# Performance work log

Measured on AMD Instinct MI355X. Metric: run time of the kernel, lower is better.

The kernel has to match this reference:

```python
import jax, jax.numpy as jnp
import numpy as np

E = 1024          # n_embed_dim
H = 64            # head_size = n_embed_dim // n_heads (16)

def setup_inputs() -> dict:
    key = jax.random.key(0)
    k_x, k_q, k_k, k_v = jax.random.split(key, 4)
    scale = 1.0 / np.sqrt(E)
    return {
        "x": jax.random.normal(k_x, (4, 2048, E), dtype=jnp.float32),
        "ln_gamma": jnp.ones((E,), jnp.float32),
        "ln_beta": jnp.zeros((E,), jnp.float32),
        # torch nn.Linear weights: [out_features, in_features]
        "Wq": jax.random.normal(k_q, (H, E), dtype=jnp.float32) * scale,
        "Wk": jax.random.normal(k_k, (H, E), dtype=jnp.float32) * scale,
        "Wv": jax.random.normal(k_v, (H, E), dtype=jnp.float32) * scale,
    }

def reference(x, ln_gamma, ln_beta, Wq, Wk, Wv):
    # LayerNorm over last dim (eps matches torch default 1e-5)
    mu = jnp.mean(x, axis=-1, keepdims=True)
    var = jnp.mean(jnp.square(x - mu), axis=-1, keepdims=True)
    xn = (x - mu) * jax.lax.rsqrt(var + 1e-5) * ln_gamma + ln_beta

    q = jnp.einsum('bse,he->bsh', xn, Wq)   # [B,S,H]
    k = jnp.einsum('bse,he->bsh', xn, Wk)
    v = jnp.einsum('bse,he->bsh', xn, Wv)

    scores = jnp.einsum('bqh,bkh->bqk', q, k) / jnp.sqrt(jnp.float32(H))
    S = x.shape[1]
    causal = jnp.tril(jnp.ones((S, S), dtype=bool))
    scores = jnp.where(causal, scores, -jnp.inf)
    attn = jax.nn.softmax(scores, axis=-1)
    return jnp.einsum('bqk,bkh->bqh', attn, v)
```

## Files before the change

kernel.cpp:

```cpp
#include <hip/hip_runtime.h>

#define E 1024
#define HH 64
#define BB 4
#define SS 2048
#define BS (BB*SS)
#define NSLOT 144

typedef unsigned short u16;
typedef short bf16x8 __attribute__((ext_vector_type(8)));
typedef float f32x4 __attribute__((ext_vector_type(4)));

#define LOG2E_O8 0.18033688011112042f

__device__ inline u16 f2bf(float f) {
    unsigned int u = __float_as_uint(f);
    unsigned int r = (u + 0x7FFFu + ((u >> 16) & 1u)) >> 16;
    return (u16)r;
}
__device__ inline float bf2f(u16 h) {
    return __uint_as_float(((unsigned int)h) << 16);
}

__global__ __launch_bounds__(256) void ln_wcast(const float* __restrict__ x,
        const float* __restrict__ gamma, const float* __restrict__ beta,
        const float* __restrict__ Wq, const float* __restrict__ Wk,
        const float* __restrict__ Wv,
        u16* __restrict__ xn, u16* __restrict__ wc) {
    const int t = threadIdx.x;
    if (blockIdx.x < 2048) {
        const int w = t >> 6, lane = t & 63;
        const size_t row = (size_t)blockIdx.x * 4 + w;
        const float4* xr = (const float4*)(x + row * E);
        float4 v[4];
        #pragma unroll
        for (int i = 0; i < 4; ++i) v[i] = xr[lane + 64 * i];
        float s = 0.f, sq = 0.f;
        #pragma unroll
        for (int i = 0; i < 4; ++i) {
            s  += v[i].x + v[i].y + v[i].z + v[i].w;
            sq += v[i].x*v[i].x + v[i].y*v[i].y + v[i].z*v[i].z + v[i].w*v[i].w;
        }
        #pragma unroll
        for (int off = 32; off > 0; off >>= 1) {
            s  += __shfl_xor(s,  off);
            sq += __shfl_xor(sq, off);
        }
        const float mean = s * (1.0f / E);
        const float var  = sq * (1.0f / E) - mean * mean;
        const float rstd = rsqrtf(var + 1e-5f);
        const float4* gr = (const float4*)gamma;
        const float4* br = (const float4*)beta;
        #pragma unroll
        for (int i = 0; i < 4; ++i) {
            const float4 g  = gr[lane + 64 * i];
            const float4 bt = br[lane + 64 * i];
            ushort4 o;
            o.x = f2bf((v[i].x - mean) * rstd * g.x + bt.x);
            o.y = f2bf((v[i].y - mean) * rstd * g.y + bt.y);
            o.z = f2bf((v[i].z - mean) * rstd * g.z + bt.z);
            o.w = f2bf((v[i].w - mean) * rstd * g.w + bt.w);
            *(ushort4*)(xn + row * E + (lane + 64 * i) * 4) = o;
        }
    } else {
        const int row = blockIdx.x - 2048;
        const float* src = (row < 64)  ? (Wq + (size_t)row * E)
                         : (row < 128) ? (Wk + (size_t)(row - 64) * E)
                                       : (Wv + (size_t)(row - 128) * E);
        const float sc = (row < 64) ? LOG2E_O8 : 1.0f;
        const float4 v = *(const float4*)(src + t * 4);
        ushort4 o;
        o.x = f2bf(v.x * sc); o.y = f2bf(v.y * sc);
        o.z = f2bf(v.z * sc); o.w = f2bf(v.w * sc);
        *(ushort4*)(wc + (size_t)row * E + t * 4) = o;
    }
}

__global__ __launch_bounds__(256) void qkv_mfma(const u16* __restrict__ xn,
        const u16* __restrict__ wc,
        u16* __restrict__ qb, u16* __restrict__ kb, u16* __restrict__ vt) {
    const int mb   = blockIdx.x >> 1;
    const int half = blockIdx.x & 1;
    const int row0 = mb * 32;
    const int t = threadIdx.x;
    const int w = t >> 6, lane = t & 63;
    const int quad = lane >> 4, r15 = lane & 15;
    const int mt = w >> 1, cgrp = w & 1;
    __shared__ u16 Xs[32 * 128];
    __shared__ u16 Ws[96 * 128];
    f32x4 acc[3] = {};
    const int xrow = mt * 16 + r15;

    for (int kc8 = 0; kc8 < 8; ++kc8) {
        __syncthreads();
        {
            const int row = t >> 3, ch = t & 7;
            #pragma unroll
            for (int hf = 0; hf < 2; ++hf) {
                const uint4 d = *(const uint4*)(xn + (size_t)(row0 + row) * E
                                                + kc8 * 128 + hf * 64 + ch * 8);
                *(uint4*)&Xs[row * 128 + hf * 64 + (ch ^ (row & 7)) * 8] = d;
            }
        }
        #pragma unroll
        for (int i = 0; i < 6; ++i) {
            const int idx = i * 256 + t;
            const int wl = idx >> 4, ch16 = idx & 15;
            const int hf = ch16 >> 3, ch = ch16 & 7;
            const uint4 d = *(const uint4*)(wc + (size_t)(half * 96 + wl) * E
                                            + kc8 * 128 + hf * 64 + ch * 8);
            *(uint4*)&Ws[wl * 128 + hf * 64 + (ch ^ (wl & 7)) * 8] = d;
        }
        __syncthreads();
        #pragma unroll
        for (int kk = 0; kk < 4; ++kk) {
            const int hf = kk >> 1, q4 = (kk & 1) * 4 + quad;
            const bf16x8 af = *(const bf16x8*)&Xs[xrow * 128 + hf * 64 + (q4 ^ (xrow & 7)) * 8];
            #pragma unroll
            for (int j = 0; j < 3; ++j) {
                const int wl = (cgrp * 3 + j) * 16 + r15;
                const bf16x8 bfr = *(const bf16x8*)&Ws[wl * 128 + hf * 64 + (q4 ^ (wl & 7)) * 8];
                acc[j] = __builtin_amdgcn_mfma_f32_16x16x32_bf16(af, bfr, acc[j], 0, 0, 0);
            }
        }
    }
    const int b    = row0 >> 11;
    const int key0 = row0 & 2047;
    #pragma unroll
    for (int j = 0; j < 3; ++j) {
        const int cg  = half * 96 + cgrp * 48 + j * 16 + r15;
        const int sel = cg >> 6;
        const int col = cg & 63;
        if (sel < 2) {
            u16* base = (sel == 0) ? qb : kb;
            #pragma unroll
            for (int r = 0; r < 4; ++r) {
                const size_t row = (size_t)row0 + mt * 16 + quad * 4 + r;
                base[row * HH + col] = f2bf(acc[j][r]);
            }
        } else {
            ushort4 pk;
            pk.x = f2bf(acc[j][0]); pk.y = f2bf(acc[j][1]);
            pk.z = f2bf(acc[j][2]); pk.w = f2bf(acc[j][3]);
            *(ushort4*)(vt + (size_t)b * HH * SS + (size_t)col * SS
                           + key0 + mt * 16 + quad * 4) = pk;
        }
    }
}

__global__ __launch_bounds__(256) void attn_partial(const u16* __restrict__ qb,
        const u16* __restrict__ kb, const u16* __restrict__ vt,
        u16* __restrict__ po, float* __restrict__ pl,
        float* __restrict__ out) {
    const int bid = blockIdx.x;
    const int b   = bid >> 8;
    const int rem = bid & 255;
    const int qt  = rem >> 3, c = rem & 7;
    const int a   = qt >> 2;
    if (c > a) return;
    const int nc   = a + 1;
    const int r_   = qt & 3;
    const int slot = b * NSLOT + 2 * a * (a + 1) + r_ * (a + 1) + c;
    const int q0   = qt << 6;
    const int t = threadIdx.x;
    const int w = t >> 6, lane = t & 63;
    const int quad = lane >> 4, r15 = lane & 15;

    __shared__ u16 Ks[4 * 64 * 64];
    __shared__ u16 VT[4 * 64 * 64];
    __shared__ u16 Ps[64 * 64];

    const size_t qrow = ((size_t)b * SS + q0 + w * 16 + r15) * HH;
    const bf16x8 qf0 = *(const bf16x8*)(qb + qrow + quad * 8);
    const bf16x8 qf1 = *(const bf16x8*)(qb + qrow + 32 + quad * 8);

    const int ntiles = min(c * 4 + 4, qt + 1) - c * 4;

    {
        const int row = t >> 2, ch0 = (t & 3) * 2;
        for (int tl = 0; tl < ntiles; ++tl) {
            const int kt = (c * 4 + tl) << 6;
            const uint4* srcK = (const uint4*)(kb + ((size_t)b * SS + kt + row) * HH + ch0 * 8);
            const uint4 k0 = srcK[0], k1 = srcK[1];
            *(uint4*)&Ks[tl * 4096 + row * 64 + ((ch0    ) ^ (row & 7)) * 8] = k0;
            *(uint4*)&Ks[tl * 4096 + row * 64 + ((ch0 + 1) ^ (row & 7)) * 8] = k1;
            const uint4* srcV = (const uint4*)(vt + (size_t)b * HH * SS + (size_t)row * SS
                                               + kt + ch0 * 8);
            const uint4 v0 = srcV[0], v1 = srcV[1];
            *(uint4*)&VT[tl * 4096 + row * 64 + ((ch0    ) ^ (row & 7)) * 8] = v0;
            *(uint4*)&VT[tl * 4096 + row * 64 + ((ch0 + 1) ^ (row & 7)) * 8] = v1;
        }
    }
    __syncthreads();

    f32x4 o[4] = {};
    float l_[4] = {0.f, 0.f, 0.f, 0.f};

    for (int tl = 0; tl < ntiles; ++tl) {
        const int tile = c * 4 + tl;
        const u16* KsT = &Ks[tl * 4096];
        const u16* VTT = &VT[tl * 4096];

        f32x4 s[4] = {};
        #pragma unroll
        for (int nt = 0; nt < 4; ++nt) {
            const int krow = nt * 16 + r15;
            const bf16x8 k0 = *(const bf16x8*)&KsT[krow * 64 + ((    quad) ^ (krow & 7)) * 8];
            const bf16x8 k1 = *(const bf16x8*)&KsT[krow * 64 + ((4 + quad) ^ (krow & 7)) * 8];
            s[nt] = __builtin_amdgcn_mfma_f32_16x16x32_bf16(qf0, k0, s[nt], 0, 0, 0);
            s[nt] = __builtin_amdgcn_mfma_f32_16x16x32_bf16(qf1, k1, s[nt], 0, 0, 0);
        }
        if (tile == qt) {
            #pragma unroll
            for (int nt = 0; nt < 4; ++nt)
                #pragma unroll
                for (int r = 0; r < 4; ++r)
                    if (nt * 16 + r15 > w * 16 + quad * 4 + r) s[nt][r] = -INFINITY;
        }

        float p[4][4];
        #pragma unroll
        for (int r = 0; r < 4; ++r) {
            #pragma unroll
            for (int nt = 0; nt < 4; ++nt)
                p[nt][r] = __builtin_amdgcn_exp2f(s[nt][r]);
            l_[r] += (p[0][r] + p[1][r]) + (p[2][r] + p[3][r]);
        }

        #pragma unroll
        for (int nt = 0; nt < 4; ++nt)
            #pragma unroll
            for (int r = 0; r < 4; ++r) {
                const int prow = w * 16 + quad * 4 + r;
                const int col  = nt * 16 + r15;
                Ps[prow * 64 + (((col >> 3) ^ (prow & 7)) * 8) + (col & 7)] = f2bf(p[nt][r]);
            }
        const int arow = w * 16 + r15;
        const bf16x8 pf0 = *(const bf16x8*)&Ps[arow * 64 + ((    quad) ^ (arow & 7)) * 8];
        const bf16x8 pf1 = *(const bf16x8*)&Ps[arow * 64 + ((4 + quad) ^ (arow & 7)) * 8];

        #pragma unroll
        for (int ht = 0; ht < 4; ++ht) {
            const int vrow = ht * 16 + r15;
            const bf16x8 v0 = *(const bf16x8*)&VTT[vrow * 64 + ((    quad) ^ (vrow & 7)) * 8];
            const bf16x8 v1 = *(const bf16x8*)&VTT[vrow * 64 + ((4 + quad) ^ (vrow & 7)) * 8];
            o[ht] = __builtin_amdgcn_mfma_f32_16x16x32_bf16(pf0, v0, o[ht], 0, 0, 0);
            o[ht] = __builtin_amdgcn_mfma_f32_16x16x32_bf16(pf1, v1, o[ht], 0, 0, 0);
        }
    }

    #pragma unroll
    for (int r = 0; r < 4; ++r) {
        l_[r] += __shfl_xor(l_[r], 1); l_[r] += __shfl_xor(l_[r], 2);
        l_[r] += __shfl_xor(l_[r], 4); l_[r] += __shfl_xor(l_[r], 8);
    }

    if (nc == 1) {
        #pragma unroll
        for (int r = 0; r < 4; ++r) {
            const float inv = 1.0f / l_[r];
            const size_t orow = ((size_t)b * SS + q0 + w * 16 + quad * 4 + r) * HH;
            #pragma unroll
            for (int ht = 0; ht < 4; ++ht)
                out[orow + ht * 16 + r15] = o[ht][r] * inv;
        }
        return;
    }
    #pragma unroll
    for (int r = 0; r < 4; ++r) {
        const int q = w * 16 + quad * 4 + r;
        #pragma unroll
        for (int ht = 0; ht < 4; ++ht)
            po[(size_t)slot * 4096 + q * 64 + ht * 16 + r15] = f2bf(o[ht][r]);
        if (r15 == 0) pl[slot * 64 + q] = l_[r];
    }
}

__global__ __launch_bounds__(256) void attn_reduce(const u16* __restrict__ po,
        const float* __restrict__ pl, float* __restrict__ out) {
    const int bid = blockIdx.x;
    const int b = bid >> 7, rem = bid & 127;
    const int qt = rem >> 2, qq = rem & 3;
    if (qt < 4) return;
    const int a = qt >> 2, r_ = qt & 3;
    const int nc = a + 1;
    const int sbase = b * NSLOT + 2 * a * (a + 1) + r_ * (a + 1);
    const int t = threadIdx.x;
    const int h = t & 63, qr = t >> 6;
    #pragma unroll
    for (int i = 0; i < 4; ++i) {
        const int q = qq * 16 + qr * 4 + i;
        float osum = 0.f, lsum = 0.f;
        for (int cidx = 0; cidx < nc; ++cidx) {
            osum += bf2f(po[(size_t)(sbase + cidx) * 4096 + q * 64 + h]);
            lsum += pl[(sbase + cidx) * 64 + q];
        }
        out[((size_t)b * SS + (qt << 6) + q) * HH + h] = osum / lsum;
    }
}

extern "C" void kernel_launch(void* const* d_in, const int* in_sizes, int n_in,
                              void* d_out, int out_size, void* d_ws, size_t ws_size,
                              hipStream_t stream) {
    const float* x     = (const float*)d_in[0];
    const float* gamma = (const float*)d_in[1];
    const float* beta  = (const float*)d_in[2];
    const float* Wq    = (const float*)d_in[3];
    const float* Wk    = (const float*)d_in[4];
    const float* Wv    = (const float*)d_in[5];
    float* out = (float*)d_out;

    char* p = (char*)d_ws;
    u16*   xn   = (u16*)p;                         p += (size_t)BS * E * 2;
    u16*   wc   = (u16*)p;                         p += 393216;
    u16*   qb   = (u16*)p;                         p += (size_t)BS * HH * 2;
    u16*   kb   = (u16*)p;                         p += (size_t)BS * HH * 2;
    u16*   vt   = (u16*)p;                         p += (size_t)BS * HH * 2;
    u16*   po   = (u16*)p;                         p += (size_t)BB * NSLOT * 4096 * 2;
    float* pl   = (float*)p;

    ln_wcast    <<<2048 + 192,  256, 0, stream>>>(x, gamma, beta, Wq, Wk, Wv, xn, wc);
    qkv_mfma    <<<BS / 16,     256, 0, stream>>>(xn, wc, qb, kb, vt);
    attn_partial<<<BB * 32 * 8, 256, 0, stream>>>(qb, kb, vt, po, pl, out);
    attn_reduce <<<BB * 32 * 4, 256, 0, stream>>>(po, pl, out);
}
```

Measured before the change: 121.3 us.

## Fuse LayerNorm normalization into QKV projection and fold gamma/beta into weights

The first kernel now computes only per-row mean and rstd instead of writing a normalized bf16 copy of x. The QKV GEMM reads fp32 x directly and normalizes while staging tiles into shared memory. Gamma is folded into the bf16 weights and beta becomes a per-output bias added in the epilogue. This removes the 16 MB bf16 xn write and re-read, but x is read twice in fp32 (32 MB each time), and each tile load now does conversion arithmetic.

```diff
diff --git a/kernel.cpp b/kernel.cpp
--- a/kernel.cpp
+++ b/kernel.cpp
@@ -22,45 +22,35 @@
     return __uint_as_float(((unsigned int)h) << 16);
 }
 
-__global__ __launch_bounds__(256) void ln_wcast(const float* __restrict__ x,
+__global__ __launch_bounds__(256) void stats_wcast(const float* __restrict__ x,
         const float* __restrict__ gamma, const float* __restrict__ beta,
         const float* __restrict__ Wq, const float* __restrict__ Wk,
         const float* __restrict__ Wv,
-        u16* __restrict__ xn, u16* __restrict__ wc) {
+        float* __restrict__ smu, float* __restrict__ srs,
+        u16* __restrict__ wc, float* __restrict__ bias) {
+    __shared__ float red[4];
     const int t = threadIdx.x;
     if (blockIdx.x < 2048) {
         const int w = t >> 6, lane = t & 63;
         const size_t row = (size_t)blockIdx.x * 4 + w;
         const float4* xr = (const float4*)(x + row * E);
-        float4 v[4];
-        #pragma unroll
-        for (int i = 0; i < 4; ++i) v[i] = xr[lane + 64 * i];
         float s = 0.f, sq = 0.f;
         #pragma unroll
         for (int i = 0; i < 4; ++i) {
-            s  += v[i].x + v[i].y + v[i].z + v[i].w;
-            sq += v[i].x*v[i].x + v[i].y*v[i].y + v[i].z*v[i].z + v[i].w*v[i].w;
+            const float4 v = xr[lane + 64 * i];
+            s  += v.x + v.y + v.z + v.w;
+            sq += v.x*v.x + v.y*v.y + v.z*v.z + v.w*v.w;
         }
         #pragma unroll
         for (int off = 32; off > 0; off >>= 1) {
             s  += __shfl_xor(s,  off);
             sq += __shfl_xor(sq, off);
         }
-        const float mean = s * (1.0f / E);
-        const float var  = sq * (1.0f / E) - mean * mean;
-        const float rstd = rsqrtf(var + 1e-5f);
-        const float4* gr = (const float4*)gamma;
-        const float4* br = (const float4*)beta;
-        #pragma unroll
-        for (int i = 0; i < 4; ++i) {
-            const float4 g  = gr[lane + 64 * i];
-            const float4 bt = br[lane + 64 * i];
-            ushort4 o;
-            o.x = f2bf((v[i].x - mean) * rstd * g.x + bt.x);
-            o.y = f2bf((v[i].y - mean) * rstd * g.y + bt.y);
-            o.z = f2bf((v[i].z - mean) * rstd * g.z + bt.z);
-            o.w = f2bf((v[i].w - mean) * rstd * g.w + bt.w);
-            *(ushort4*)(xn + row * E + (lane + 64 * i) * 4) = o;
+        if (lane == 0) {
+            const float mean = s * (1.0f / E);
+            const float var  = sq * (1.0f / E) - mean * mean;
+            smu[row] = mean;
+            srs[row] = rsqrtf(var + 1e-5f);
         }
     } else {
         const int row = blockIdx.x - 2048;
@@ -69,15 +59,25 @@
                                        : (Wv + (size_t)(row - 128) * E);
         const float sc = (row < 64) ? LOG2E_O8 : 1.0f;
         const float4 v = *(const float4*)(src + t * 4);
+        const float4 g = *(const float4*)(gamma + t * 4);
+        const float4 b = *(const float4*)(beta  + t * 4);
         ushort4 o;
-        o.x = f2bf(v.x * sc); o.y = f2bf(v.y * sc);
-        o.z = f2bf(v.z * sc); o.w = f2bf(v.w * sc);
+        o.x = f2bf(v.x * g.x * sc); o.y = f2bf(v.y * g.y * sc);
+        o.z = f2bf(v.z * g.z * sc); o.w = f2bf(v.w * g.w * sc);
         *(ushort4*)(wc + (size_t)row * E + t * 4) = o;
-    }
-}
-
-__global__ __launch_bounds__(256) void qkv_mfma(const u16* __restrict__ xn,
-        const u16* __restrict__ wc,
+
+        float s = (v.x * b.x + v.y * b.y + v.z * b.z + v.w * b.w) * sc;
+        #pragma unroll
+        for (int off = 32; off > 0; off >>= 1) s += __shfl_xor(s, off);
+        if ((t & 63) == 0) red[t >> 6] = s;
+        __syncthreads();
+        if (t == 0) bias[row] = red[0] + red[1] + red[2] + red[3];
+    }
+}
+
+__global__ __launch_bounds__(256) void qkv_mfma(const float* __restrict__ x,
+        const float* __restrict__ smu, const float* __restrict__ srs,
+        const u16* __restrict__ wc, const float* __restrict__ bias,
         u16* __restrict__ qb, u16* __restrict__ kb, u16* __restrict__ vt) {
     const int mb   = blockIdx.x >> 1;
     const int half = blockIdx.x & 1;
@@ -91,15 +91,29 @@
     f32x4 acc[3] = {};
     const int xrow = mt * 16 + r15;
 
+    const int srow = t >> 3, sch = t & 7;
+    const float mu = smu[row0 + srow];
+    const float rs = srs[row0 + srow];
+    const float* xsrc = x + (size_t)(row0 + srow) * E;
+
+    float bj[3];
+    #pragma unroll
+    for (int j = 0; j < 3; ++j) bj[j] = bias[half * 96 + cgrp * 48 + j * 16 + r15];
+
     for (int kc8 = 0; kc8 < 8; ++kc8) {
         __syncthreads();
         {
-            const int row = t >> 3, ch = t & 7;
             #pragma unroll
             for (int hf = 0; hf < 2; ++hf) {
-                const uint4 d = *(const uint4*)(xn + (size_t)(row0 + row) * E
-                                                + kc8 * 128 + hf * 64 + ch * 8);
-                *(uint4*)&Xs[row * 128 + hf * 64 + (ch ^ (row & 7)) * 8] = d;
+                const float* sp = xsrc + kc8 * 128 + hf * 64 + sch * 8;
+                const float4 f0 = *(const float4*)sp;
+                const float4 f1 = *(const float4*)(sp + 4);
+                u16 tmp[8];
+                tmp[0] = f2bf((f0.x - mu) * rs); tmp[1] = f2bf((f0.y - mu) * rs);
+                tmp[2] = f2bf((f0.z - mu) * rs); tmp[3] = f2bf((f0.w - mu) * rs);
+                tmp[4] = f2bf((f1.x - mu) * rs); tmp[5] = f2bf((f1.y - mu) * rs);
+                tmp[6] = f2bf((f1.z - mu) * rs); tmp[7] = f2bf((f1.w - mu) * rs);
+                *(uint4*)&Xs[srow * 128 + hf * 64 + (sch ^ (srow & 7)) * 8] = *(uint4*)tmp;
             }
         }
         #pragma unroll
@@ -136,12 +150,12 @@
             #pragma unroll
             for (int r = 0; r < 4; ++r) {
                 const size_t row = (size_t)row0 + mt * 16 + quad * 4 + r;
-                base[row * HH + col] = f2bf(acc[j][r]);
+                base[row * HH + col] = f2bf(acc[j][r] + bj[j]);
             }
         } else {
             ushort4 pk;
-            pk.x = f2bf(acc[j][0]); pk.y = f2bf(acc[j][1]);
-            pk.z = f2bf(acc[j][2]); pk.w = f2bf(acc[j][3]);
+            pk.x = f2bf(acc[j][0] + bj[j]); pk.y = f2bf(acc[j][1] + bj[j]);
+            pk.z = f2bf(acc[j][2] + bj[j]); pk.w = f2bf(acc[j][3] + bj[j]);
             *(ushort4*)(vt + (size_t)b * HH * SS + (size_t)col * SS
                            + key0 + mt * 16 + quad * 4) = pk;
         }
@@ -311,16 +325,19 @@
     float* out = (float*)d_out;
 
     char* p = (char*)d_ws;
-    u16*   xn   = (u16*)p;                         p += (size_t)BS * E * 2;
+    float* smu  = (float*)p;                       p += (size_t)BS * 4;
+    float* srs  = (float*)p;                       p += (size_t)BS * 4;
     u16*   wc   = (u16*)p;                         p += 393216;
+    float* bias = (float*)p;                       p += 1024;
     u16*   qb   = (u16*)p;                         p += (size_t)BS * HH * 2;
     u16*   kb   = (u16*)p;                         p += (size_t)BS * HH * 2;
     u16*   vt   = (u16*)p;                         p += (size_t)BS * HH * 2;
     u16*   po   = (u16*)p;                         p += (size_t)BB * NSLOT * 4096 * 2;
     float* pl   = (float*)p;
 
-    ln_wcast    <<<2048 + 192,  256, 0, stream>>>(x, gamma, beta, Wq, Wk, Wv, xn, wc);
-    qkv_mfma    <<<BS / 16,     256, 0, stream>>>(xn, wc, qb, kb, vt);
+    stats_wcast <<<2048 + 192,  256, 0, stream>>>(x, gamma, beta, Wq, Wk, Wv,
+                                                  smu, srs, wc, bias);
+    qkv_mfma    <<<BS / 16,     256, 0, stream>>>(x, smu, srs, wc, bias, qb, kb, vt);
     attn_partial<<<BB * 32 * 8, 256, 0, stream>>>(qb, kb, vt, po, pl, out);
     attn_reduce <<<BB * 32 * 4, 256, 0, stream>>>(po, pl, out);
 }
```

New measurement: 125.3 us. 3.3% more time.
